# Kernel optimization log

Measured on AMD Instinct MI355X. Metric: run time of the kernel, lower is better.

The kernel has to match this reference:

```python
import jax, jax.numpy as jnp
import numpy as np

B, S, D, H = 8, 1024, 1024, 16
DH = D // H
LN_EPS = 1e-5
SLOPE = 0.01  # nn.LeakyReLU default negative_slope


def _ln(x, g, b):
    m = x.mean(-1, keepdims=True)
    v = ((x - m) ** 2).mean(-1, keepdims=True)
    return (x - m) / jnp.sqrt(v + LN_EPS) * g + b


def _leaky(x):
    return jnp.where(x >= 0, x, SLOPE * x)


def setup_inputs() -> dict:
    key = jax.random.key(0)
    ks = jax.random.split(key, 6)
    q = jax.random.normal(ks[0], (B, S, D), dtype=jnp.float32)
    masks = jnp.ones((B, S), dtype=jnp.int32)  # all-valid mask (masked_fill is a no-op)
    w1 = jax.random.normal(ks[1], (D, D), dtype=jnp.float32) * 0.02
    b1 = jnp.zeros((D,), jnp.float32)
    w2 = jax.random.normal(ks[2], (D, D), dtype=jnp.float32) * 0.02
    b2 = jnp.zeros((D,), jnp.float32)
    ones = jnp.ones((D,), jnp.float32)
    zeros = jnp.zeros((D,), jnp.float32)
    return dict(q=q, masks=masks,
                w1=w1, b1=b1, ln1_g=ones, ln1_b=zeros,
                w2=w2, b2=b2, ln2_g=ones, ln2_b=zeros,
                anf_g=ones, anf_b=zeros,
                an1_g=ones, an1_b=zeros,
                an2_g=ones, an2_b=zeros)


def reference(q, masks, w1, b1, ln1_g, ln1_b, w2, b2, ln2_g, ln2_b,
              anf_g, anf_b, an1_g, an1_b, an2_g, an2_b):
    # --- multi-head cosine-similarity attention (k = v = q, no projections) ---
    qh = q.reshape(B, S, H, DH).transpose(0, 2, 1, 3)  # (B,H,S,DH) == separate_heads
    qn = qh / jnp.clip(jnp.linalg.norm(qh, axis=-1, keepdims=True), 1e-8)
    # cosine similarity scores, softmax over keys
    w = jax.nn.softmax(jnp.einsum('bhqd,bhkd->bhqk', qn, qn), axis=-1)
    # masked_fill AFTER softmax (faithful to source: mask per (batch, query))
    w = jnp.where(masks[:, None, :, None] == 0, jnp.float32(-1e9), w)
    heads = jnp.einsum('bhqk,bhkd->bhqd', w, qh)
    attn = heads.transpose(0, 2, 1, 3).reshape(B, S, D)  # concat_heads
    # --- add_norm1 (dropout=0.5 but eval mode => identity) ---
    y1 = _ln(q + attn, an1_g, an1_b)
    # --- PositionWiseFFN: Linear->LN->LeakyReLU x2, then internal AddNorm ---
    h = _leaky(_ln(y1 @ w1 + b1, ln1_g, ln1_b))
    y = _leaky(_ln(h @ w2 + b2, ln2_g, ln2_b))
    y2 = _ln(y1 + y, anf_g, anf_b)
    # --- add_norm2 ---
    return _ln(y1 + y2, an2_g, an2_b)
```

## Files before the change

### kernel.cpp

```cpp
#include <hip/hip_runtime.h>
#include <hip/hip_bf16.h>

#define BB 8
#define SS 1024
#define DD 1024
#define HH 16

typedef __attribute__((ext_vector_type(8))) short short8;
typedef __attribute__((ext_vector_type(8))) __bf16 bf16x8;
typedef __attribute__((ext_vector_type(4))) float f32x4;

__device__ inline float bf2f(unsigned short h){
  unsigned u = ((unsigned)h) << 16;
  return __builtin_bit_cast(float, u);
}
__device__ inline unsigned short f2bf(float f){
  unsigned u = __builtin_bit_cast(unsigned, f);
  u += 0x7fffu + ((u >> 16) & 1u);
  return (unsigned short)(u >> 16);
}
__device__ inline f32x4 mfma16(short8 a, short8 b, f32x4 c){
  return __builtin_amdgcn_mfma_f32_16x16x32_bf16(
      __builtin_bit_cast(bf16x8, a), __builtin_bit_cast(bf16x8, b), c, 0, 0, 0);
}
__device__ inline void gld_lds16(const unsigned short* g, unsigned short* l){
  __builtin_amdgcn_global_load_lds((const __attribute__((address_space(1))) void*)g,
      (__attribute__((address_space(3))) void*)l, 16, 0, 0);
}

__global__ __launch_bounds__(256) void prep_w(const float* __restrict__ w1,
                                              const float* __restrict__ w2,
                                              unsigned short* __restrict__ w1T,
                                              unsigned short* __restrict__ w2T){
  __shared__ float tile[64][65];
  const float* src = blockIdx.z ? w2 : w1;
  unsigned short* dst = blockIdx.z ? w2T : w1T;
  int k0 = blockIdx.x * 64, n0 = blockIdx.y * 64;
  int tx = threadIdx.x & 63, ty = threadIdx.x >> 6;
#pragma unroll
  for (int r = 0; r < 16; ++r)
    tile[ty + 4*r][tx] = src[(k0 + ty + 4*r) * DD + n0 + tx];
  __syncthreads();
#pragma unroll
  for (int r = 0; r < 16; ++r)
    dst[(n0 + ty + 4*r) * DD + k0 + tx] = f2bf(tile[tx][ty + 4*r]);
}

__global__ __launch_bounds__(256) void prep_q(const float* __restrict__ q,
                                              unsigned short* __restrict__ kf,
                                              unsigned short* __restrict__ vf,
                                              unsigned short* __restrict__ qb){
  __shared__ float tile[64][65];
  __shared__ float rinv[64];
  int bh = blockIdx.x >> 4, st = blockIdx.x & 15;
  int b = bh >> 4, h = bh & 15;
  int t = threadIdx.x;
  int tx = t & 63, ty = t >> 6;
  int srow = b * SS + st * 64;
#pragma unroll
  for (int r = 0; r < 16; ++r)
    tile[ty + 4*r][tx] = q[(size_t)(srow + ty + 4*r) * DD + h * 64 + tx];
  __syncthreads();
  {
    int s = t >> 2, p = t & 3;
    float ssum = 0.f;
#pragma unroll
    for (int i = 0; i < 16; ++i){ float v = tile[s][p*16 + i]; ssum += v * v; }
    ssum += __shfl_xor(ssum, 1);
    ssum += __shfl_xor(ssum, 2);
    if (p == 0) rinv[s] = 1.0f / fmaxf(sqrtf(ssum), 1e-8f);
  }
  __syncthreads();
#pragma unroll
  for (int r = 0; r < 16; ++r)
    qb[(size_t)(srow + ty + 4*r) * DD + h * 64 + tx] = f2bf(tile[ty + 4*r][tx]);
#pragma unroll
  for (int v = 0; v < 2; ++v){
    int idx = t * 2 + v;
    int c_l = idx >> 6, lane = idx & 63;
    int g2 = c_l >> 2, c = (c_l >> 1) & 1, hf = c_l & 1;
    int lrq = lane & 15, lgq = lane >> 4;
    int s = g2 * 32 + (lrq >> 2) * 8 + c * 4 + (lrq & 3);
    int d0 = hf * 32 + lgq * 8;
    float rv = rinv[s] * 1.20112240878645f;
    short8 o;
#pragma unroll
    for (int e = 0; e < 8; ++e) o[e] = (short)f2bf(tile[s][d0 + e] * rv);
    *(short8*)(kf + ((size_t)(bh * 128 + st * 8 + c_l) * 64 + lane) * 8) = o;
  }
#pragma unroll
  for (int v = 0; v < 2; ++v){
    int idx = t * 2 + v;
    int kt2 = idx >> 8, db = (idx >> 6) & 3, lane = idx & 63;
    int d = db * 16 + (lane & 15);
    int k0 = kt2 * 32 + (lane >> 4) * 8;
    short8 o;
#pragma unroll
    for (int e = 0; e < 8; ++e) o[e] = (short)f2bf(tile[k0 + e][d]);
    *(short8*)(vf + ((size_t)((bh * 32 + st * 2 + kt2) * 4 + db) * 512 + lane * 8)) = o;
  }
}

#define NPH 16
__global__ __launch_bounds__(512, 4) void attn_kern(const unsigned short* __restrict__ kf,
                                                    const unsigned short* __restrict__ vf,
                                                    const int* __restrict__ masks,
                                                    unsigned short* __restrict__ attnb){
  __shared__ unsigned short Kb[3][8][512];
  __shared__ unsigned short Vb[3][8][512];
  __shared__ int anym;
  const int bh = blockIdx.x, b = bh >> 4, h = bh & 15;
  const int by = blockIdx.y;
  const int t = threadIdx.x, w = t >> 6, l = t & 63;
  const int lr = l & 15, lg = l >> 4;
  if (t == 0) anym = 0;
  __syncthreads();
  if (t < 256 && masks[b * SS + by * 256 + t] == 0) anym = 1;

  short8 aQ[2][2];
#pragma unroll
  for (int c = 0; c < 2; ++c)
#pragma unroll
    for (int hf = 0; hf < 2; ++hf)
      aQ[c][hf] = *(const short8*)(kf +
          ((size_t)(bh * 128 + (by * 8 + w) * 4 + c * 2 + hf) * 64 + l) * 8);

  const short ONEB = (short)0x3F80;
  const short8 ones = {ONEB, ONEB, ONEB, ONEB, ONEB, ONEB, ONEB, ONEB};

#define STAGE(ph, bf) do {                                                            \
    if (w < 4){                                                                       \
      gld_lds16(kf + ((size_t)(bh * 128 + (2*(ph)) * 4 + w) * 64 + l) * 8,            \
                &Kb[bf][w][0]);                                                       \
      gld_lds16(kf + ((size_t)(bh * 128 + (2*(ph)+1) * 4 + w) * 64 + l) * 8,          \
                &Kb[bf][4 + w][0]);                                                   \
    } else {                                                                          \
      gld_lds16(vf + ((size_t)((bh * 32 + 2*(ph)) * 4 + (w - 4)) * 512 + l * 8),      \
                &Vb[bf][w - 4][0]);                                                   \
      gld_lds16(vf + ((size_t)((bh * 32 + 2*(ph)+1) * 4 + (w - 4)) * 512 + l * 8),    \
                &Vb[bf][4 + (w - 4)][0]);                                             \
    }                                                                                 \
  } while (0)

  STAGE(0, 0);
  STAGE(1, 1);
  asm volatile("s_waitcnt vmcnt(2) lgkmcnt(0)" ::: "memory");
  __builtin_amdgcn_s_barrier();

  f32x4 o[2][4] = {};
  f32x4 rsacc[2] = {};

  for (int ph = 0; ph < NPH; ++ph){
    const int cur = ph % 3;
    if (ph + 2 < NPH) STAGE(ph + 2, (ph + 2) % 3);
#pragma unroll
    for (int gi = 0; gi < 2; ++gi){
      short8 bK[2][2];
#pragma unroll
      for (int c = 0; c < 2; ++c)
#pragma unroll
        for (int hf = 0; hf < 2; ++hf)
          bK[c][hf] = *(const short8*)&Kb[cur][gi * 4 + c * 2 + hf][l * 8];
      f32x4 sc[2][2];
#pragma unroll
      for (int qc = 0; qc < 2; ++qc)
#pragma unroll
        for (int c = 0; c < 2; ++c){
          f32x4 z = {0.f, 0.f, 0.f, 0.f};
          z = mfma16(bK[c][0], aQ[qc][0], z);
          z = mfma16(bK[c][1], aQ[qc][1], z);
          sc[qc][c] = z;
        }
      bf16x8 pav[2];
#pragma unroll
      for (int qc = 0; qc < 2; ++qc)
#pragma unroll
        for (int c = 0; c < 2; ++c)
#pragma unroll
          for (int j = 0; j < 4; ++j){
            float x = sc[qc][c][j], pv;
            asm("v_exp_f32 %0, %1" : "=v"(pv) : "v"(x));
            pav[qc][c * 4 + j] = (__bf16)pv;
          }
      short8 pa0 = __builtin_bit_cast(short8, pav[0]);
      short8 pa1 = __builtin_bit_cast(short8, pav[1]);
      rsacc[0] = mfma16(pa0, ones, rsacc[0]);
      rsacc[1] = mfma16(pa1, ones, rsacc[1]);
#pragma unroll
      for (int db = 0; db < 4; ++db){
        short8 bV = *(const short8*)&Vb[cur][gi * 4 + db][l * 8];
        o[0][db] = mfma16(pa0, bV, o[0][db]);
        o[1][db] = mfma16(pa1, bV, o[1][db]);
      }
    }
    if (ph + 1 < NPH){
      asm volatile("s_waitcnt lgkmcnt(0)" ::: "memory");
      if (ph + 2 < NPH) asm volatile("s_waitcnt vmcnt(2)" ::: "memory");
      else              asm volatile("s_waitcnt vmcnt(0)" ::: "memory");
      __builtin_amdgcn_s_barrier();
    }
  }

#pragma unroll
  for (int qc = 0; qc < 2; ++qc){
    float invj[4];
#pragma unroll
    for (int j = 0; j < 4; ++j) invj[j] = 1.0f / rsacc[qc][j];
#pragma unroll
    for (int db = 0; db < 4; ++db)
#pragma unroll
      for (int j = 0; j < 4; ++j){
        int qrow = by * 256 + w * 32 + lg * 8 + qc * 4 + j;
        float val = o[qc][db][j] * invj[j];
        if (anym && masks[b * SS + qrow] == 0){
          float vs = 0.f;
          for (int kt = 0; kt < 32; ++kt)
            for (int lgp = 0; lgp < 4; ++lgp){
              const unsigned short* vp = vf +
                  ((size_t)((bh * 32 + kt) * 4 + db) * 512 + (lgp * 16 + lr) * 8);
              for (int e = 0; e < 8; ++e) vs += bf2f(vp[e]);
            }
          val = -1e9f * vs;
        }
        attnb[(size_t)(b * SS + qrow) * DD + h * 64 + db * 16 + lr] = f2bf(val);
      }
  }
#undef STAGE
}

__device__ inline float2 block_reduce2(float a, float bq){
  __shared__ float sm[8];
#pragma unroll
  for (int off = 1; off < 64; off <<= 1){
    a += __shfl_xor(a, off);
    bq += __shfl_xor(bq, off);
  }
  int w = threadIdx.x >> 6;
  if ((threadIdx.x & 63) == 0){ sm[2*w] = a; sm[2*w + 1] = bq; }
  __syncthreads();
  float2 r;
  r.x = sm[0] + sm[2] + sm[4] + sm[6];
  r.y = sm[1] + sm[3] + sm[5] + sm[7];
  __syncthreads();
  return r;
}

__global__ __launch_bounds__(256) void addnorm1(const unsigned short* __restrict__ qb,
                                                const unsigned short* __restrict__ attnb,
                                                const float* __restrict__ g,
                                                const float* __restrict__ bt,
                                                unsigned short* __restrict__ y1b){
  int row = blockIdx.x, t = threadIdx.x;
  ushort4 qv = *(const ushort4*)(qb + (size_t)row * DD + t * 4);
  ushort4 av = *(const ushort4*)(attnb + (size_t)row * DD + t * 4);
  float x[4] = { bf2f(qv.x) + bf2f(av.x), bf2f(qv.y) + bf2f(av.y),
                 bf2f(qv.z) + bf2f(av.z), bf2f(qv.w) + bf2f(av.w) };
  float s = 0.f, ssq = 0.f;
#pragma unroll
  for (int i = 0; i < 4; ++i){ s += x[i]; ssq += x[i] * x[i]; }
  float2 r = block_reduce2(s, ssq);
  float m = r.x * (1.0f / DD);
  float rs = rsqrtf(r.y * (1.0f / DD) - m * m + 1e-5f);
  float4 gv = *(const float4*)(g + t * 4);
  float4 bv = *(const float4*)(bt + t * 4);
  float y[4] = { (x[0]-m)*rs*gv.x + bv.x, (x[1]-m)*rs*gv.y + bv.y,
                 (x[2]-m)*rs*gv.z + bv.z, (x[3]-m)*rs*gv.w + bv.w };
  ushort4 ob = { f2bf(y[0]), f2bf(y[1]), f2bf(y[2]), f2bf(y[3]) };
  *(ushort4*)(y1b + (size_t)row * DD + t * 4) = ob;
}

__global__ __launch_bounds__(256, 2) void gemm_bias(const unsigned short* __restrict__ X,
                                                    const unsigned short* __restrict__ WT,
                                                    const float* __restrict__ bias,
                                                    unsigned short* __restrict__ out){
  __shared__ unsigned short As[3][128 * 32];
  __shared__ unsigned short Bs[3][128 * 32];
  int t = threadIdx.x, l = t & 63, w = t >> 6;
  int wm = w >> 1, wn = w & 1;
  int lr = l & 15, lg = l >> 4;
  int id = blockIdx.x;
  int bm = (((id & 7) << 3) + ((id >> 3) & 7)) * 128;
  int bn = (id >> 6) * 128;
  f32x4 acc[4][4] = {};
  int r = t >> 2, cb = (t & 3) * 8;

#define GSTAGE(kt, bf) do {                                                        \
    gld_lds16(X  + (size_t)(bm +      r) * 1024 + (kt) * 32 + cb,                  \
              &As[bf][w * 512]);                                                   \
    gld_lds16(X  + (size_t)(bm + 64 + r) * 1024 + (kt) * 32 + cb,                  \
              &As[bf][2048 + w * 512]);                                            \
    gld_lds16(WT + (size_t)(bn +      r) * 1024 + (kt) * 32 + cb,                  \
              &Bs[bf][w * 512]);                                                   \
    gld_lds16(WT + (size_t)(bn + 64 + r) * 1024 + (kt) * 32 + cb,                  \
              &Bs[bf][2048 + w * 512]);                                            \
  } while (0)

  GSTAGE(0, 0);
  GSTAGE(1, 1);
  asm volatile("s_waitcnt vmcnt(4)" ::: "memory");
  __builtin_amdgcn_s_barrier();

  for (int kt = 0; kt < 32; ++kt){
    const int cur = kt % 3;
    if (kt + 2 < 32) GSTAGE(kt + 2, (kt + 2) % 3);
    short8 aA[4], bB[4];
#pragma unroll
    for (int i = 0; i < 4; ++i)
      aA[i] = *(const short8*)&As[cur][(wm * 64 + i * 16 + lr) * 32 + lg * 8];
#pragma unroll
    for (int i = 0; i < 4; ++i)
      bB[i] = *(const short8*)&Bs[cur][(wn * 64 + i * 16 + lr) * 32 + lg * 8];
#pragma unroll
    for (int mi = 0; mi < 4; ++mi)
#pragma unroll
      for (int ni = 0; ni < 4; ++ni)
        acc[mi][ni] = mfma16(aA[mi], bB[ni], acc[mi][ni]);
    if (kt + 1 < 32){
      asm volatile("s_waitcnt lgkmcnt(0)" ::: "memory");
      if (kt + 2 < 32) asm volatile("s_waitcnt vmcnt(4)" ::: "memory");
      else             asm volatile("s_waitcnt vmcnt(0)" ::: "memory");
      __builtin_amdgcn_s_barrier();
    }
  }
#undef GSTAGE
#pragma unroll
  for (int ni = 0; ni < 4; ++ni){
    int col = bn + wn * 64 + ni * 16 + lr;
    float bv = bias[col];
#pragma unroll
    for (int mi = 0; mi < 4; ++mi){
      int row0 = bm + wm * 64 + mi * 16 + lg * 4;
#pragma unroll
      for (int j = 0; j < 4; ++j)
        out[(size_t)(row0 + j) * 1024 + col] = f2bf(acc[mi][ni][j] + bv);
    }
  }
}

__global__ __launch_bounds__(256) void ln_leaky(const unsigned short* __restrict__ in,
                                                const float* __restrict__ g,
                                                const float* __restrict__ bt,
                                                unsigned short* __restrict__ out){
  int row = blockIdx.x, t = threadIdx.x;
  ushort4 iv = *(const ushort4*)(in + (size_t)row * DD + t * 4);
  float x[4] = { bf2f(iv.x), bf2f(iv.y), bf2f(iv.z), bf2f(iv.w) };
  float s = 0.f, ssq = 0.f;
#pragma unroll
  for (int i = 0; i < 4; ++i){ s += x[i]; ssq += x[i] * x[i]; }
  float2 r = block_reduce2(s, ssq);
  float m = r.x * (1.0f / DD);
  float rs = rsqrtf(r.y * (1.0f / DD) - m * m + 1e-5f);
  float4 gv = *(const float4*)(g + t * 4);
  float4 bv = *(const float4*)(bt + t * 4);
  ushort4 ov;
  {
    float v0 = (x[0]-m)*rs*gv.x + bv.x; v0 = v0 >= 0.f ? v0 : 0.01f*v0; ov.x = f2bf(v0);
    float v1 = (x[1]-m)*rs*gv.y + bv.y; v1 = v1 >= 0.f ? v1 : 0.01f*v1; ov.y = f2bf(v1);
    float v2 = (x[2]-m)*rs*gv.z + bv.z; v2 = v2 >= 0.f ? v2 : 0.01f*v2; ov.z = f2bf(v2);
    float v3 = (x[3]-m)*rs*gv.w + bv.w; v3 = v3 >= 0.f ? v3 : 0.01f*v3; ov.w = f2bf(v3);
  }
  *(ushort4*)(out + (size_t)row * DD + t * 4) = ov;
}

__global__ __launch_bounds__(256) void final_kern(const unsigned short* __restrict__ g2,
                                                  const unsigned short* __restrict__ y1,
                                                  const float* __restrict__ ln2g, const float* __restrict__ ln2b,
                                                  const float* __restrict__ anfg, const float* __restrict__ anfb,
                                                  const float* __restrict__ an2g, const float* __restrict__ an2b,
                                                  float* __restrict__ out){
  int row = blockIdx.x, t = threadIdx.x;
  ushort4 iv = *(const ushort4*)(g2 + (size_t)row * DD + t * 4);
  ushort4 y1v = *(const ushort4*)(y1 + (size_t)row * DD + t * 4);
  float x[4] = { bf2f(iv.x), bf2f(iv.y), bf2f(iv.z), bf2f(iv.w) };
  float yy1[4] = { bf2f(y1v.x), bf2f(y1v.y), bf2f(y1v.z), bf2f(y1v.w) };
  float s = 0.f, ssq = 0.f;
#pragma unroll
  for (int i = 0; i < 4; ++i){ s += x[i]; ssq += x[i]*x[i]; }
  float2 r = block_reduce2(s, ssq);
  float m = r.x * (1.0f / DD);
  float rs = rsqrtf(r.y * (1.0f / DD) - m*m + 1e-5f);
  float4 gv = *(const float4*)(ln2g + t * 4);
  float4 bv = *(const float4*)(ln2b + t * 4);
  float y[4] = { (x[0]-m)*rs*gv.x + bv.x, (x[1]-m)*rs*gv.y + bv.y,
                 (x[2]-m)*rs*gv.z + bv.z, (x[3]-m)*rs*gv.w + bv.w };
#pragma unroll
  for (int i = 0; i < 4; ++i) y[i] = y[i] >= 0.f ? y[i] : 0.01f*y[i];

  float tv[4]; s = 0.f; ssq = 0.f;
#pragma unroll
  for (int i = 0; i < 4; ++i){ tv[i] = yy1[i] + y[i]; s += tv[i]; ssq += tv[i]*tv[i]; }
  r = block_reduce2(s, ssq);
  m = r.x * (1.0f / DD);
  rs = rsqrtf(r.y * (1.0f / DD) - m*m + 1e-5f);
  gv = *(const float4*)(anfg + t * 4);
  bv = *(const float4*)(anfb + t * 4);
  float y2[4] = { (tv[0]-m)*rs*gv.x + bv.x, (tv[1]-m)*rs*gv.y + bv.y,
                  (tv[2]-m)*rs*gv.z + bv.z, (tv[3]-m)*rs*gv.w + bv.w };

  float u[4]; s = 0.f; ssq = 0.f;
#pragma unroll
  for (int i = 0; i < 4; ++i){ u[i] = yy1[i] + y2[i]; s += u[i]; ssq += u[i]*u[i]; }
  r = block_reduce2(s, ssq);
  m = r.x * (1.0f / DD);
  rs = rsqrtf(r.y * (1.0f / DD) - m*m + 1e-5f);
  gv = *(const float4*)(an2g + t * 4);
  bv = *(const float4*)(an2b + t * 4);
  float4 ov = { (u[0]-m)*rs*gv.x + bv.x, (u[1]-m)*rs*gv.y + bv.y,
                (u[2]-m)*rs*gv.z + bv.z, (u[3]-m)*rs*gv.w + bv.w };
  *(float4*)(out + (size_t)row * DD + t * 4) = ov;
}

extern "C" void kernel_launch(void* const* d_in, const int* in_sizes, int n_in,
                              void* d_out, int out_size, void* d_ws, size_t ws_size,
                              hipStream_t stream){
  const float* q    = (const float*)d_in[0];
  const int* masks  = (const int*)d_in[1];
  const float* w1   = (const float*)d_in[2];
  const float* b1   = (const float*)d_in[3];
  const float* ln1g = (const float*)d_in[4];
  const float* ln1b = (const float*)d_in[5];
  const float* w2   = (const float*)d_in[6];
  const float* b2   = (const float*)d_in[7];
  const float* ln2g = (const float*)d_in[8];
  const float* ln2b = (const float*)d_in[9];
  const float* anfg = (const float*)d_in[10];
  const float* anfb = (const float*)d_in[11];
  const float* an1g = (const float*)d_in[12];
  const float* an1b = (const float*)d_in[13];
  const float* an2g = (const float*)d_in[14];
  const float* an2b = (const float*)d_in[15];

  char* ws = (char*)d_ws;
  unsigned short* w1T  = (unsigned short*)(ws + 0);
  unsigned short* w2T  = (unsigned short*)(ws + 2097152);
  unsigned short* kf   = (unsigned short*)(ws + 4194304);
  unsigned short* vf   = (unsigned short*)(ws + 20971520);
  unsigned short* attn = (unsigned short*)(ws + 37748736);
  unsigned short* y1b  = (unsigned short*)(ws + 54525952);
  unsigned short* qb   = (unsigned short*)(ws + 71303168);
  unsigned short* g1   = kf;
  unsigned short* hbuf = vf;
  unsigned short* g2   = attn;
  float* outp = (float*)d_out;

  prep_w<<<dim3(16, 16, 2), 256, 0, stream>>>(w1, w2, w1T, w2T);
  prep_q<<<dim3(2048), 256, 0, stream>>>(q, kf, vf, qb);
  attn_kern<<<dim3(128, 4), 512, 0, stream>>>(kf, vf, masks, attn);
  addnorm1<<<dim3(8192), 256, 0, stream>>>(qb, attn, an1g, an1b, y1b);
  gemm_bias<<<dim3(512), 256, 0, stream>>>(y1b, w1T, b1, g1);
  ln_leaky<<<dim3(8192), 256, 0, stream>>>(g1, ln1g, ln1b, hbuf);
  gemm_bias<<<dim3(512), 256, 0, stream>>>(hbuf, w2T, b2, g2);
  final_kern<<<dim3(8192), 256, 0, stream>>>(g2, y1b, ln2g, ln2b, anfg, anfb, an2g, an2b, outp);
}
```

Before: 155.0 us.

## Load K/V fragments directly from global memory instead of LDS triple-buffering

The attention kernel drops its shared-memory triple-buffered K/V staging and its barriers. Each wave now reads its K and V MFMA fragments straight from global memory, relying on L2 and cache reuse across waves. Blocks shrink to 256 threads with twice as many blocks along the query axis. The shared mask pre-check is removed, so every thread reads the mask per row. This removes LDS traffic and synchronisation but adds redundant global and L2 reads of K/V across waves, and global load latency now sits directly on the loop.

```diff
diff --git a/kernel.cpp b/kernel.cpp
--- a/kernel.cpp
+++ b/kernel.cpp
@@ -101,21 +101,15 @@
   }
 }
 
-#define NPH 16
-__global__ __launch_bounds__(512, 4) void attn_kern(const unsigned short* __restrict__ kf,
+__global__ __launch_bounds__(256, 3) void attn_kern(const unsigned short* __restrict__ kf,
                                                     const unsigned short* __restrict__ vf,
                                                     const int* __restrict__ masks,
                                                     unsigned short* __restrict__ attnb){
-  __shared__ unsigned short Kb[3][8][512];
-  __shared__ unsigned short Vb[3][8][512];
-  __shared__ int anym;
   const int bh = blockIdx.x, b = bh >> 4, h = bh & 15;
   const int by = blockIdx.y;
   const int t = threadIdx.x, w = t >> 6, l = t & 63;
   const int lr = l & 15, lg = l >> 4;
-  if (t == 0) anym = 0;
-  __syncthreads();
-  if (t < 256 && masks[b * SS + by * 256 + t] == 0) anym = 1;
+  const int gq = by * 4 + w;
 
   short8 aQ[2][2];
 #pragma unroll
@@ -123,81 +117,57 @@
 #pragma unroll
     for (int hf = 0; hf < 2; ++hf)
       aQ[c][hf] = *(const short8*)(kf +
-          ((size_t)(bh * 128 + (by * 8 + w) * 4 + c * 2 + hf) * 64 + l) * 8);
+          ((size_t)(bh * 128 + gq * 4 + c * 2 + hf) * 64 + l) * 8);
 
   const short ONEB = (short)0x3F80;
   const short8 ones = {ONEB, ONEB, ONEB, ONEB, ONEB, ONEB, ONEB, ONEB};
 
-#define STAGE(ph, bf) do {                                                            \
-    if (w < 4){                                                                       \
-      gld_lds16(kf + ((size_t)(bh * 128 + (2*(ph)) * 4 + w) * 64 + l) * 8,            \
-                &Kb[bf][w][0]);                                                       \
-      gld_lds16(kf + ((size_t)(bh * 128 + (2*(ph)+1) * 4 + w) * 64 + l) * 8,          \
-                &Kb[bf][4 + w][0]);                                                   \
-    } else {                                                                          \
-      gld_lds16(vf + ((size_t)((bh * 32 + 2*(ph)) * 4 + (w - 4)) * 512 + l * 8),      \
-                &Vb[bf][w - 4][0]);                                                   \
-      gld_lds16(vf + ((size_t)((bh * 32 + 2*(ph)+1) * 4 + (w - 4)) * 512 + l * 8),    \
-                &Vb[bf][4 + (w - 4)][0]);                                             \
-    }                                                                                 \
-  } while (0)
-
-  STAGE(0, 0);
-  STAGE(1, 1);
-  asm volatile("s_waitcnt vmcnt(2) lgkmcnt(0)" ::: "memory");
-  __builtin_amdgcn_s_barrier();
-
   f32x4 o[2][4] = {};
   f32x4 rsacc[2] = {};
 
-  for (int ph = 0; ph < NPH; ++ph){
-    const int cur = ph % 3;
-    if (ph + 2 < NPH) STAGE(ph + 2, (ph + 2) % 3);
-#pragma unroll
-    for (int gi = 0; gi < 2; ++gi){
-      short8 bK[2][2];
+  const unsigned short* kbase = kf + (size_t)bh * 128 * 512 + (size_t)l * 8;
+  const unsigned short* vbase = vf + (size_t)bh * 32 * 2048 + (size_t)l * 8;
+
+#pragma unroll 2
+  for (int g = 0; g < 32; ++g){
+    short8 bK[2][2], bV[4];
+#pragma unroll
+    for (int c = 0; c < 2; ++c)
+#pragma unroll
+      for (int hf = 0; hf < 2; ++hf)
+        bK[c][hf] = *(const short8*)(kbase + (size_t)(g * 4 + c * 2 + hf) * 512);
+#pragma unroll
+    for (int db = 0; db < 4; ++db)
+      bV[db] = *(const short8*)(vbase + (size_t)(g * 4 + db) * 512);
+    f32x4 sc[2][2];
+#pragma unroll
+    for (int qc = 0; qc < 2; ++qc)
+#pragma unroll
+      for (int c = 0; c < 2; ++c){
+        f32x4 z = {0.f, 0.f, 0.f, 0.f};
+        z = mfma16(bK[c][0], aQ[qc][0], z);
+        z = mfma16(bK[c][1], aQ[qc][1], z);
+        sc[qc][c] = z;
+      }
+    bf16x8 pav[2];
+#pragma unroll
+    for (int qc = 0; qc < 2; ++qc)
 #pragma unroll
       for (int c = 0; c < 2; ++c)
 #pragma unroll
-        for (int hf = 0; hf < 2; ++hf)
-          bK[c][hf] = *(const short8*)&Kb[cur][gi * 4 + c * 2 + hf][l * 8];
-      f32x4 sc[2][2];
-#pragma unroll
-      for (int qc = 0; qc < 2; ++qc)
-#pragma unroll
-        for (int c = 0; c < 2; ++c){
-          f32x4 z = {0.f, 0.f, 0.f, 0.f};
-          z = mfma16(bK[c][0], aQ[qc][0], z);
-          z = mfma16(bK[c][1], aQ[qc][1], z);
-          sc[qc][c] = z;
+        for (int j = 0; j < 4; ++j){
+          float x = sc[qc][c][j], pv;
+          asm("v_exp_f32 %0, %1" : "=v"(pv) : "v"(x));
+          pav[qc][c * 4 + j] = (__bf16)pv;
         }
-      bf16x8 pav[2];
-#pragma unroll
-      for (int qc = 0; qc < 2; ++qc)
-#pragma unroll
-        for (int c = 0; c < 2; ++c)
-#pragma unroll
-          for (int j = 0; j < 4; ++j){
-            float x = sc[qc][c][j], pv;
-            asm("v_exp_f32 %0, %1" : "=v"(pv) : "v"(x));
-            pav[qc][c * 4 + j] = (__bf16)pv;
-          }
-      short8 pa0 = __builtin_bit_cast(short8, pav[0]);
-      short8 pa1 = __builtin_bit_cast(short8, pav[1]);
-      rsacc[0] = mfma16(pa0, ones, rsacc[0]);
-      rsacc[1] = mfma16(pa1, ones, rsacc[1]);
-#pragma unroll
-      for (int db = 0; db < 4; ++db){
-        short8 bV = *(const short8*)&Vb[cur][gi * 4 + db][l * 8];
-        o[0][db] = mfma16(pa0, bV, o[0][db]);
-        o[1][db] = mfma16(pa1, bV, o[1][db]);
-      }
-    }
-    if (ph + 1 < NPH){
-      asm volatile("s_waitcnt lgkmcnt(0)" ::: "memory");
-      if (ph + 2 < NPH) asm volatile("s_waitcnt vmcnt(2)" ::: "memory");
-      else              asm volatile("s_waitcnt vmcnt(0)" ::: "memory");
-      __builtin_amdgcn_s_barrier();
+    short8 pa0 = __builtin_bit_cast(short8, pav[0]);
+    short8 pa1 = __builtin_bit_cast(short8, pav[1]);
+    rsacc[0] = mfma16(pa0, ones, rsacc[0]);
+    rsacc[1] = mfma16(pa1, ones, rsacc[1]);
+#pragma unroll
+    for (int db = 0; db < 4; ++db){
+      o[0][db] = mfma16(pa0, bV[db], o[0][db]);
+      o[1][db] = mfma16(pa1, bV[db], o[1][db]);
     }
   }
 
@@ -210,9 +180,9 @@
     for (int db = 0; db < 4; ++db)
 #pragma unroll
       for (int j = 0; j < 4; ++j){
-        int qrow = by * 256 + w * 32 + lg * 8 + qc * 4 + j;
+        int qrow = by * 128 + w * 32 + lg * 8 + qc * 4 + j;
         float val = o[qc][db][j] * invj[j];
-        if (anym && masks[b * SS + qrow] == 0){
+        if (masks[b * SS + qrow] == 0){
           float vs = 0.f;
           for (int kt = 0; kt < 32; ++kt)
             for (int lgp = 0; lgp < 4; ++lgp){
@@ -225,7 +195,6 @@
         attnb[(size_t)(b * SS + qrow) * DD + h * 64 + db * 16 + lr] = f2bf(val);
       }
   }
-#undef STAGE
 }
 
 __device__ inline float2 block_reduce2(float a, float bq){
@@ -445,7 +414,7 @@
 
   prep_w<<<dim3(16, 16, 2), 256, 0, stream>>>(w1, w2, w1T, w2T);
   prep_q<<<dim3(2048), 256, 0, stream>>>(q, kf, vf, qb);
-  attn_kern<<<dim3(128, 4), 512, 0, stream>>>(kf, vf, masks, attn);
+  attn_kern<<<dim3(128, 8), 256, 0, stream>>>(kf, vf, masks, attn);
   addnorm1<<<dim3(8192), 256, 0, stream>>>(qb, attn, an1g, an1b, y1b);
   gemm_bias<<<dim3(512), 256, 0, stream>>>(y1b, w1T, b1, g1);
   ln_leaky<<<dim3(8192), 256, 0, stream>>>(g1, ln1g, ln1b, hbuf);
```

Measured after the change: 160.1 us. 3.3% more time.
